# Kernel optimization log

Measured on AMD Instinct MI355X. Metric: run time of the kernel, lower is better.

Reference implementation:

```python
import jax, jax.numpy as jnp
import numpy as np

WIDTH_IN = 8
WIDTH_OUT = 8
STRIDES = (1, 1)
PADDING = 'SAME'


def quantizer(x, width, mode='round', clip=True):
    """Fixed-point quantization to `width` bits in [-1, 1), straight-through estimator.

    mode='round' -> round-to-nearest; mode='floor' -> truncate.
    clip=True saturates to the representable range [-1, 1 - 2^-(width-1)].
    """
    scale = jnp.asarray(2.0 ** (width - 1), x.dtype)
    q = jnp.round(x * scale) if mode == 'round' else jnp.floor(x * scale)
    q = q / scale
    # straight-through: forward uses q, gradient flows as identity
    q = x + jax.lax.stop_gradient(q - x)
    if clip:
        q = jnp.clip(q, -1.0, 1.0 - 1.0 / scale)
    return q


def setup_inputs() -> dict:
    key = jax.random.key(0)
    kx, kw = jax.random.split(key)
    x = jax.random.normal(kx, (32, 112, 112, 64), dtype=jnp.float32)      # NHWC
    kernels = jax.random.normal(kw, (3, 3, 64, 128), dtype=jnp.float32) * 0.05  # HWIO, RandomNormal init
    return {"x": x, "kernels": kernels}


def reference(x, kernels):
    # Method == 'Fixed' path of MyConv2D.call
    xq = quantizer(x, WIDTH_IN, 'round', clip=True)                # quantize activations
    kq = quantizer(kernels, WIDTH_IN, 'round', clip=True)          # quantize weights
    out = jax.lax.conv_general_dilated(
        xq, kq,
        window_strides=STRIDES,
        padding=PADDING,
        dimension_numbers=('NHWC', 'HWIO', 'NHWC'),
    )                                                              # [B, 112, 112, 128]
    out = quantizer(out, WIDTH_OUT, 'floor', clip=False)           # quantize output, truncating
    return out
```

## Files before the change

kernel.cpp:

```cpp
#include <hip/hip_runtime.h>

#define NIMG 32
#define H 112
#define W 112
#define CI 64
#define CO 128

typedef __attribute__((ext_vector_type(8))) __bf16 bf16x8;
typedef __attribute__((ext_vector_type(4))) float f32x4;
typedef __attribute__((ext_vector_type(4))) short short4v;

__device__ __forceinline__ short q8bits(float v) {
    float t = rintf(v * 128.0f);
    t = fminf(fmaxf(t, -128.0f), 127.0f);
    union { float f; unsigned u; } cv; cv.f = t;
    return (short)(cv.u >> 16);
}

__global__ __launch_bounds__(256) void quant_pack_w(const float* __restrict__ w,
                                                    short* __restrict__ bp) {
    int idx = blockIdx.x * 256 + threadIdx.x;
    int j    = idx & 7;
    int lane = (idx >> 3) & 63;
    int nt   = (idx >> 9) & 7;
    int kt   = idx >> 12;
    int k = kt * 32 + (lane >> 4) * 8 + j;
    int n = nt * 16 + (lane & 15);
    bp[idx] = q8bits(w[k * CO + n]);
}

#define LDSW 114
#define LDST 72

__global__ __launch_bounds__(256, 3) void conv_kernel(const float* __restrict__ x,
                                                      const short* __restrict__ bp,
                                                      float* __restrict__ out) {
    __shared__ short xs[3 * LDSW * LDST];

    int bid = blockIdx.x;
    int n = bid / H;
    int h = bid - n * H;
    int tid = threadIdx.x;

    const float* xin = x + (size_t)n * (H * W * CI);
    for (int r = 0; r < 3; ++r) {
        int hr = h + r - 1;
        bool rowok = ((unsigned)hr < (unsigned)H);
        const float* srow = xin + (size_t)hr * (W * CI);
        for (int t = tid; t < LDSW * 16; t += 256) {
            int c = t >> 4;
            int ci4 = (t & 15) << 2;
            int wcol = c - 1;
            float4 v = {0.0f, 0.0f, 0.0f, 0.0f};
            if (rowok && (unsigned)wcol < (unsigned)W) {
                v = *(const float4*)&srow[wcol * CI + ci4];
            }
            short4v sv;
            sv.x = q8bits(v.x); sv.y = q8bits(v.y);
            sv.z = q8bits(v.z); sv.w = q8bits(v.w);
            *(short4v*)&xs[(r * LDSW + c) * LDST + ci4] = sv;
        }
    }
    __syncthreads();

    int lane = tid & 63;
    int wave = tid >> 6;
    int laneoff = (lane & 15) * LDST + (lane >> 4) * 8;

    const bf16x8* bfr = (const bf16x8*)bp;
    int nt0 = wave * 2;

    f32x4 acc[7][2];
    #pragma unroll
    for (int mt = 0; mt < 7; ++mt) {
        acc[mt][0] = (f32x4){0.f, 0.f, 0.f, 0.f};
        acc[mt][1] = (f32x4){0.f, 0.f, 0.f, 0.f};
    }

    #pragma unroll
    for (int kk = 0; kk < 18; ++kk) {
        int rs = kk >> 1;
        int r = rs / 3;
        int s = rs - r * 3;
        bf16x8 b0 = bfr[(kk * 8 + nt0    ) * 64 + lane];
        bf16x8 b1 = bfr[(kk * 8 + nt0 + 1) * 64 + lane];
        int abase = (r * LDSW + s) * LDST + (kk & 1) * 32 + laneoff;
        #pragma unroll
        for (int mt = 0; mt < 7; ++mt) {
            bf16x8 a = *(const bf16x8*)&xs[abase + mt * 16 * LDST];
            acc[mt][0] = __builtin_amdgcn_mfma_f32_16x16x32_bf16(a, b0, acc[mt][0], 0, 0, 0);
            acc[mt][1] = __builtin_amdgcn_mfma_f32_16x16x32_bf16(a, b1, acc[mt][1], 0, 0, 0);
        }
    }

    float* orow = out + (size_t)(n * H + h) * (W * CO);
    int colc = wave * 32 + (lane & 15);
    int rowb = (lane >> 4) * 4;
    #pragma unroll
    for (int mt = 0; mt < 7; ++mt) {
        #pragma unroll
        for (int t2 = 0; t2 < 2; ++t2) {
            int co = colc + t2 * 16;
            #pragma unroll
            for (int rg = 0; rg < 4; ++rg) {
                int m = mt * 16 + rowb + rg;
                float sv = acc[mt][t2][rg];
                orow[m * CO + co] = floorf(sv * 0.0078125f) * 0.0078125f;
            }
        }
    }
}

extern "C" void kernel_launch(void* const* d_in, const int* in_sizes, int n_in,
                              void* d_out, int out_size, void* d_ws, size_t ws_size,
                              hipStream_t stream) {
    const float* x = (const float*)d_in[0];
    const float* w = (const float*)d_in[1];
    float* out = (float*)d_out;
    short* bp = (short*)d_ws;

    quant_pack_w<<<288, 256, 0, stream>>>(w, bp);
    conv_kernel<<<NIMG * H, 256, 0, stream>>>(x, bp, out);
}
```

Baseline: 343.3 us.

## Pre-quantize input to bf16 and compute two output rows per block with direct-to-LDS loads

Measured after the change: 333.3 us. 2.9% less time.

```diff
diff --git a/kernel.cpp b/kernel.cpp
--- a/kernel.cpp
+++ b/kernel.cpp
@@ -9,6 +9,7 @@
 typedef __attribute__((ext_vector_type(8))) __bf16 bf16x8;
 typedef __attribute__((ext_vector_type(4))) float f32x4;
 typedef __attribute__((ext_vector_type(4))) short short4v;
+typedef __attribute__((ext_vector_type(4))) int int4v;
 
 __device__ __forceinline__ short q8bits(float v) {
     float t = rintf(v * 128.0f);
@@ -29,32 +30,137 @@
     bp[idx] = q8bits(w[k * CO + n]);
 }
 
+__global__ __launch_bounds__(256) void quant_x(const float* __restrict__ x,
+                                               short* __restrict__ xq) {
+    size_t i = ((size_t)blockIdx.x * 256 + threadIdx.x) * 8;
+    float4 v0 = *(const float4*)&x[i];
+    float4 v1 = *(const float4*)&x[i + 4];
+    short4v a, b;
+    a.x = q8bits(v0.x); a.y = q8bits(v0.y); a.z = q8bits(v0.z); a.w = q8bits(v0.w);
+    b.x = q8bits(v1.x); b.y = q8bits(v1.y); b.z = q8bits(v1.z); b.w = q8bits(v1.w);
+    *(short4v*)&xq[i]     = a;
+    *(short4v*)&xq[i + 4] = b;
+}
+
+#define LROW 7296
+
+__global__ __launch_bounds__(256, 2) void conv2(const short* __restrict__ xq,
+                                                const short* __restrict__ bp,
+                                                float* __restrict__ out) {
+    __shared__ short xs[4 * LROW];
+    int bid = blockIdx.x;
+    int n  = bid / 56;
+    int hp = bid - n * 56;
+    int h0 = hp * 2;
+    int tid  = threadIdx.x;
+    int lane = tid & 63;
+    int wave = tid >> 6;
+
+    short* ldsrow = &xs[wave * LROW];
+    int hr = h0 - 1 + wave;
+    if ((unsigned)hr < (unsigned)H) {
+        const short* grow = xq + ((size_t)(n * H + hr) * W) * CI;
+        int lc = lane >> 3;
+        int jp = lane & 7;
+        #pragma unroll
+        for (int i = 0; i < 14; ++i) {
+            int gc = i * 8 + lc;
+            int jl = jp ^ ((gc + 1) & 7);
+            const short* g = grow + gc * 64 + jl * 8;
+            __builtin_amdgcn_global_load_lds(
+                (const __attribute__((address_space(1))) void*)g,
+                (__attribute__((address_space(3))) void*)(ldsrow + 64 + i * 512),
+                16, 0, 0);
+        }
+    } else {
+        for (int t = lane; t < 912; t += 64)
+            *(int4v*)&ldsrow[t * 8] = (int4v){0, 0, 0, 0};
+    }
+    if (lane < 16) {
+        int c = (lane & 8) ? 113 : 0;
+        *(int4v*)&ldsrow[c * 64 + (lane & 7) * 8] = (int4v){0, 0, 0, 0};
+    }
+    __syncthreads();
+
+    int lane15  = lane & 15;
+    int hi      = lane >> 4;
+    int row_sel = wave >> 1;
+    int nt0     = (wave & 1) * 4;
+
+    const bf16x8* bfr = (const bf16x8*)bp;
+
+    f32x4 acc[7][4];
+    #pragma unroll
+    for (int mt = 0; mt < 7; ++mt)
+        #pragma unroll
+        for (int t = 0; t < 4; ++t)
+            acc[mt][t] = (f32x4){0.f, 0.f, 0.f, 0.f};
+
+    #pragma unroll
+    for (int r = 0; r < 3; ++r) {
+        int rbase = (row_sel + r) * LROW;
+        #pragma unroll
+        for (int s = 0; s < 3; ++s) {
+            int cb = s + lane15;
+            int sx = cb & 7;
+            int abase = rbase + cb * 64;
+            #pragma unroll
+            for (int kh = 0; kh < 2; ++kh) {
+                int kk = (r * 3 + s) * 2 + kh;
+                bf16x8 b0 = bfr[(kk * 8 + nt0    ) * 64 + lane];
+                bf16x8 b1 = bfr[(kk * 8 + nt0 + 1) * 64 + lane];
+                bf16x8 b2 = bfr[(kk * 8 + nt0 + 2) * 64 + lane];
+                bf16x8 b3 = bfr[(kk * 8 + nt0 + 3) * 64 + lane];
+                int joff = ((kh * 4 + hi) ^ sx) * 8;
+                #pragma unroll
+                for (int mt = 0; mt < 7; ++mt) {
+                    bf16x8 a = *(const bf16x8*)&xs[abase + mt * 1024 + joff];
+                    acc[mt][0] = __builtin_amdgcn_mfma_f32_16x16x32_bf16(a, b0, acc[mt][0], 0, 0, 0);
+                    acc[mt][1] = __builtin_amdgcn_mfma_f32_16x16x32_bf16(a, b1, acc[mt][1], 0, 0, 0);
+                    acc[mt][2] = __builtin_amdgcn_mfma_f32_16x16x32_bf16(a, b2, acc[mt][2], 0, 0, 0);
+                    acc[mt][3] = __builtin_amdgcn_mfma_f32_16x16x32_bf16(a, b3, acc[mt][3], 0, 0, 0);
+                }
+            }
+        }
+    }
+
+    float* orow = out + (size_t)((n * H + h0 + row_sel) * W) * CO;
+    int co0  = (wave & 1) * 64 + lane15;
+    int rowb = hi * 4;
+    #pragma unroll
+    for (int mt = 0; mt < 7; ++mt)
+        #pragma unroll
+        for (int t = 0; t < 4; ++t)
+            #pragma unroll
+            for (int rg = 0; rg < 4; ++rg) {
+                int m = mt * 16 + rowb + rg;
+                orow[m * CO + co0 + t * 16] =
+                    floorf(acc[mt][t][rg] * 0.0078125f) * 0.0078125f;
+            }
+}
+
 #define LDSW 114
 #define LDST 72
-
-__global__ __launch_bounds__(256, 3) void conv_kernel(const float* __restrict__ x,
-                                                      const short* __restrict__ bp,
-                                                      float* __restrict__ out) {
+__global__ __launch_bounds__(256, 3) void conv_fb(const float* __restrict__ x,
+                                                  const short* __restrict__ bp,
+                                                  float* __restrict__ out) {
     __shared__ short xs[3 * LDSW * LDST];
-
     int bid = blockIdx.x;
     int n = bid / H;
     int h = bid - n * H;
     int tid = threadIdx.x;
-
     const float* xin = x + (size_t)n * (H * W * CI);
     for (int r = 0; r < 3; ++r) {
-        int hr = h + r - 1;
-        bool rowok = ((unsigned)hr < (unsigned)H);
-        const float* srow = xin + (size_t)hr * (W * CI);
+        int hrow = h + r - 1;
+        bool rowok = ((unsigned)hrow < (unsigned)H);
+        const float* srow = xin + (size_t)hrow * (W * CI);
         for (int t = tid; t < LDSW * 16; t += 256) {
             int c = t >> 4;
             int ci4 = (t & 15) << 2;
             int wcol = c - 1;
-            float4 v = {0.0f, 0.0f, 0.0f, 0.0f};
-            if (rowok && (unsigned)wcol < (unsigned)W) {
+            float4 v = {0.f, 0.f, 0.f, 0.f};
+            if (rowok && (unsigned)wcol < (unsigned)W)
                 v = *(const float4*)&srow[wcol * CI + ci4];
-            }
             short4v sv;
             sv.x = q8bits(v.x); sv.y = q8bits(v.y);
             sv.z = q8bits(v.z); sv.w = q8bits(v.w);
@@ -62,21 +168,17 @@
         }
     }
     __syncthreads();
-
     int lane = tid & 63;
     int wave = tid >> 6;
     int laneoff = (lane & 15) * LDST + (lane >> 4) * 8;
-
     const bf16x8* bfr = (const bf16x8*)bp;
     int nt0 = wave * 2;
-
     f32x4 acc[7][2];
     #pragma unroll
     for (int mt = 0; mt < 7; ++mt) {
         acc[mt][0] = (f32x4){0.f, 0.f, 0.f, 0.f};
         acc[mt][1] = (f32x4){0.f, 0.f, 0.f, 0.f};
     }
-
     #pragma unroll
     for (int kk = 0; kk < 18; ++kk) {
         int rs = kk >> 1;
@@ -92,23 +194,19 @@
             acc[mt][1] = __builtin_amdgcn_mfma_f32_16x16x32_bf16(a, b1, acc[mt][1], 0, 0, 0);
         }
     }
-
     float* orow = out + (size_t)(n * H + h) * (W * CO);
     int colc = wave * 32 + (lane & 15);
     int rowb = (lane >> 4) * 4;
     #pragma unroll
-    for (int mt = 0; mt < 7; ++mt) {
-        #pragma unroll
-        for (int t2 = 0; t2 < 2; ++t2) {
-            int co = colc + t2 * 16;
+    for (int mt = 0; mt < 7; ++mt)
+        #pragma unroll
+        for (int t2 = 0; t2 < 2; ++t2)
             #pragma unroll
             for (int rg = 0; rg < 4; ++rg) {
                 int m = mt * 16 + rowb + rg;
-                float sv = acc[mt][t2][rg];
-                orow[m * CO + co] = floorf(sv * 0.0078125f) * 0.0078125f;
+                orow[m * CO + colc + t2 * 16] =
+                    floorf(acc[mt][t2][rg] * 0.0078125f) * 0.0078125f;
             }
-        }
-    }
 }
 
 extern "C" void kernel_launch(void* const* d_in, const int* in_sizes, int n_in,
@@ -117,8 +215,17 @@
     const float* x = (const float*)d_in[0];
     const float* w = (const float*)d_in[1];
     float* out = (float*)d_out;
+
     short* bp = (short*)d_ws;
-
+    const size_t BP_BYTES = 147456;
+    const size_t XQ_BYTES = (size_t)NIMG * H * W * CI * 2;
     quant_pack_w<<<288, 256, 0, stream>>>(w, bp);
-    conv_kernel<<<NIMG * H, 256, 0, stream>>>(x, bp, out);
-}
+
+    if (ws_size >= BP_BYTES + XQ_BYTES) {
+        short* xqp = (short*)((char*)d_ws + BP_BYTES);
+        quant_x<<<12544, 256, 0, stream>>>(x, xqp);
+        conv2<<<NIMG * 56, 256, 0, stream>>>(xqp, bp, out);
+    } else {
+        conv_fb<<<NIMG * H, 256, 0, stream>>>(x, bp, out);
+    }
+}
```
